# Kernel tuning notes

Hardware: AMD Instinct MI355X
Metric: run time of the kernel (lower is better)

Reference implementation:

```python
import jax, jax.numpy as jnp
import numpy as np

EPS = 1e-7
MAX_NORM = 10.0  # safe_expmap tangent-norm clamp


def _sinh_div(d):
    # sinh(d)/d, stable at d->0
    ds = jnp.maximum(d, 1e-6)
    return jnp.where(d < 1e-6, 1.0, jnp.sinh(ds) / ds)


def _div_sinh(d):
    # d/sinh(d), stable at d->0
    ds = jnp.maximum(d, 1e-6)
    return jnp.where(d < 1e-6, 1.0, ds / jnp.sinh(ds))


def projx(x):
    # re-project onto hyperboloid: x0 = sqrt(1 + ||x_spatial||^2)
    sp = x[..., 1:]
    x0 = jnp.sqrt(1.0 + jnp.sum(sp * sp, -1, keepdims=True))
    return jnp.concatenate([x0, sp], -1)


def logmap0(x):
    # log map at origin o=(1,0,...,0); tangent has first coord 0
    x0 = jnp.clip(x[..., :1], 1.0 + EPS, None)
    d = jnp.arccosh(x0)
    v_sp = _div_sinh(d) * x[..., 1:]
    return jnp.concatenate([jnp.zeros_like(x0), v_sp], -1)


def safe_expmap0(v):
    # exp map at origin with norm clamping for stability
    sp = v[..., 1:]
    n = jnp.sqrt(jnp.sum(sp * sp, -1, keepdims=True))
    scale = jnp.minimum(1.0, MAX_NORM / jnp.maximum(n, EPS))
    sp = sp * scale
    m = jnp.minimum(n, MAX_NORM)
    return jnp.concatenate([jnp.cosh(m), _sinh_div(m) * sp], -1)


def lorentz_inner(x, y):
    return -x[..., :1] * y[..., :1] + jnp.sum(x[..., 1:] * y[..., 1:], -1, keepdims=True)


def logmap(x, y):
    ip = jnp.clip(lorentz_inner(x, y), None, -(1.0 + EPS))
    d = jnp.arccosh(-ip)
    return _div_sinh(d) * (y + ip * x)


def safe_expmap(x, v):
    # exp map at x with Lorentz-norm clamping
    vv = lorentz_inner(v, v)
    n = jnp.sqrt(jnp.clip(vv, 0.0, None))
    scale = jnp.minimum(1.0, MAX_NORM / jnp.maximum(n, EPS))
    v = v * scale
    m = jnp.minimum(n, MAX_NORM)
    return jnp.cosh(m) * x + _sinh_div(m) * v


def lorentz_linear(x_hyp, W, b):
    # Lorentz -> tangent -> linear -> Lorentz
    y_tan = logmap0(x_hyp) @ W.T + b
    return projx(safe_expmap0(y_tan))


def setup_inputs() -> dict:
    key = jax.random.key(0)
    ks = jax.random.split(key, 8)
    N, D, H = 32768, 256, 1024
    z_sp = 0.5 * jax.random.normal(ks[0], (N, D - 1), dtype=jnp.float32)
    z_h = projx(jnp.concatenate([jnp.zeros((N, 1), jnp.float32), z_sp], -1))
    s = lambda fi, fo: (2.0 / (fi + fo)) ** 0.5
    return {
        "z_h": z_h,
        "w0": s(D, H) * jax.random.normal(ks[1], (H, D), dtype=jnp.float32),
        "b0": jnp.zeros((H,), jnp.float32),
        "w1": s(H, H) * jax.random.normal(ks[2], (H, H), dtype=jnp.float32),
        "b1": jnp.zeros((H,), jnp.float32),
        "w2": s(H, D) * jax.random.normal(ks[3], (D, H), dtype=jnp.float32),
        "b2": jnp.zeros((D,), jnp.float32),
        "alpha": jnp.float32(0.7),
        "step_size": jnp.float32(1.0),
    }


def reference(z_h, w0, b0, w1, b1, w2, b2, alpha, step_size):
    # v_tangent branch: x_previous is None, average_velocity is None
    v_tangent = logmap0(z_h)
    v_hyp = projx(safe_expmap0(v_tangent))

    # LorentzMLP (n_layers=2 -> 3 LorentzLinear layers); dropout is identity (eval)
    x = v_hyp
    for W, b in ((w0, b0), (w1, b1)):
        x = lorentz_linear(x, W, b)
        x = projx(safe_expmap0(logmap0(x)))
    v_transformed_hyp = lorentz_linear(x, w2, b2)

    v_transformed = logmap0(v_transformed_hyp)
    step = jax.nn.sigmoid(step_size)
    v_final = step * v_transformed
    z_update = projx(safe_expmap(z_h, v_final))

    a = jax.nn.sigmoid(alpha)
    tangent_direction = logmap(z_h, z_update)
    scaled_tangent = (1.0 - a) * tangent_direction
    z_next = projx(safe_expmap(z_h, scaled_tangent))
    return (z_next, z_h)
```

## Files before the change

### kernel.cpp

```cpp
#include <hip/hip_runtime.h>
#include <math.h>

#define EPSF 1e-7f
#define MAXN 10.0f

typedef unsigned short ushortT;
typedef __bf16 bf16_8 __attribute__((ext_vector_type(8)));
typedef float f32_4 __attribute__((ext_vector_type(4)));

#define MFMA16 __builtin_amdgcn_mfma_f32_16x16x32_bf16
#define BAR asm volatile("s_barrier" ::: "memory")

__device__ __forceinline__ float sinh_div_f(float d) {
    float ds = fmaxf(d, 1e-6f);
    return (d < 1e-6f) ? 1.0f : sinhf(ds) / ds;
}
__device__ __forceinline__ float div_sinh_f(float d) {
    float ds = fmaxf(d, 1e-6f);
    return (d < 1e-6f) ? 1.0f : ds / sinhf(ds);
}
__device__ __forceinline__ float wred(float v) {
#pragma unroll
    for (int off = 32; off > 0; off >>= 1) v += __shfl_xor(v, off, 64);
    return v;
}
__device__ __forceinline__ void bsplit(float x, ushortT& h, ushortT& l) {
    unsigned u = __float_as_uint(x);
    unsigned r = (u + 0x7fffu + ((u >> 16) & 1u)) >> 16;
    h = (ushortT)r;
    float lo = x - __uint_as_float(r << 16);
    unsigned ul = __float_as_uint(lo);
    l = (ushortT)((ul + 0x7fffu + ((ul >> 16) & 1u)) >> 16);
}
__device__ __forceinline__ void gload_lds16(const void* g, void* l) {
    __builtin_amdgcn_global_load_lds(
        (const __attribute__((address_space(1))) unsigned int*)g,
        (__attribute__((address_space(3))) unsigned int*)l, 16, 0, 0);
}

__global__ void split_kernel(const float* __restrict__ x, ushortT* __restrict__ hi,
                             ushortT* __restrict__ lo, int n4) {
    int idx = blockIdx.x * blockDim.x + threadIdx.x;
    if (idx >= n4) return;
    float4 v = reinterpret_cast<const float4*>(x)[idx];
    float f[4] = {v.x, v.y, v.z, v.w};
    ushortT hh[4], ll[4];
#pragma unroll
    for (int e = 0; e < 4; ++e) bsplit(f[e], hh[e], ll[e]);
    reinterpret_cast<ushort4*>(hi)[idx] = ushort4{hh[0], hh[1], hh[2], hh[3]};
    reinterpret_cast<ushort4*>(lo)[idx] = ushort4{ll[0], ll[1], ll[2], ll[3]};
}

__global__ void prep_kernel(const float* __restrict__ z, ushortT* __restrict__ th,
                            ushortT* __restrict__ tl, int N) {
    int gw = (blockIdx.x * blockDim.x + threadIdx.x) >> 6;
    int lane = threadIdx.x & 63;
    if (gw >= N) return;
    float4 zv = reinterpret_cast<const float4*>(z + (size_t)gw * 256)[lane];
    float z0 = __shfl(zv.x, 0, 64);
    float x0 = fmaxf(z0, 1.f + EPSF);
    float d = acoshf(x0);
    float f = div_sinh_f(d);
    float vx = (lane == 0) ? 0.f : zv.x * f;
    float vy = zv.y * f, vz = zv.z * f, vw = zv.w * f;
    float ss = wred(vx * vx + vy * vy + vz * vz + vw * vw);
    float n = sqrtf(ss);
    float s = fminf(1.f, MAXN / fmaxf(n, EPSF));
    float o[4] = {vx * s, vy * s, vz * s, vw * s};
    ushortT hh[4], ll[4];
#pragma unroll
    for (int e = 0; e < 4; ++e) bsplit(o[e], hh[e], ll[e]);
    reinterpret_cast<ushort4*>(th + (size_t)gw * 256)[lane] = ushort4{hh[0], hh[1], hh[2], hh[3]};
    reinterpret_cast<ushort4*>(tl + (size_t)gw * 256)[lane] = ushort4{ll[0], ll[1], ll[2], ll[3]};
}

__global__ void rowscale_kernel(const float* __restrict__ partials, float* __restrict__ scale,
                                int N, int nSlices) {
    int r = blockIdx.x * blockDim.x + threadIdx.x;
    if (r >= N) return;
    float s = 0.f;
    for (int k = 0; k < nSlices; ++k) s += partials[(size_t)k * N + r];
    float n = sqrtf(s);
    scale[r] = fminf(1.f, MAXN / fmaxf(n, EPSF));
}

template<int OUTMODE, int IM>
__global__ __launch_bounds__(512, 2) void gemm_v4(
    const ushortT* __restrict__ Ah_g, const ushortT* __restrict__ Al_g,
    const ushortT* __restrict__ Wh_g, const ushortT* __restrict__ Wl_g,
    const float* __restrict__ bias, const float* __restrict__ scaleA,
    float* __restrict__ outF, ushortT* __restrict__ outH, ushortT* __restrict__ outL,
    float* __restrict__ partials, int K, int M, int nColBlk, int Nrows)
{
    constexpr int BM = IM * 32;
    constexpr int AS = BM * 32;
    constexpr int BS = 256 * 32;
    constexpr int BUF = 2 * AS + 2 * BS;
    constexpr int HM = IM / 2;
    __shared__ __align__(16) ushortT lds[2 * BUF];

    const int tid = threadIdx.x;
    const int wid = tid >> 6, lane = tid & 63;
    const int nwg = gridDim.x;
    const int swz = ((int)blockIdx.x & 7) * (nwg >> 3) + ((int)blockIdx.x >> 3);
    const int rb = swz / nColBlk, cb = swz % nColBlk;
    const int rowBase = rb * BM, colBase = cb * 256;

    const int rl = tid >> 2;
    const int ks = (tid & 3) ^ ((rl >> 1) & 3);
    const int d8 = tid * 8;
    const ushortT* gAh0 = Ah_g + (size_t)(rowBase + rl) * K + ks * 8;
    const ushortT* gAl0 = Al_g + (size_t)(rowBase + rl) * K + ks * 8;
    const ushortT* gAh1 = Ah_g + (size_t)(rowBase + 128 + rl) * K + ks * 8;
    const ushortT* gAl1 = Al_g + (size_t)(rowBase + 128 + rl) * K + ks * 8;
    const ushortT* gBh0 = Wh_g + (size_t)(colBase + rl) * K + ks * 8;
    const ushortT* gBh1 = Wh_g + (size_t)(colBase + 128 + rl) * K + ks * 8;
    const ushortT* gBl0 = Wl_g + (size_t)(colBase + rl) * K + ks * 8;
    const ushortT* gBl1 = Wl_g + (size_t)(colBase + 128 + rl) * K + ks * 8;
#define STG(p, dst, nbo, nk) gload_lds16((p) + (nk), &lds[(nbo) + (dst) + d8])

    const int warpM = wid >> 2, warpN = wid & 3;
    const int frow = lane & 15, fk = lane >> 4;
    const int pslot8 = (fk ^ ((frow >> 1) & 3)) * 8;
    const int aoff = (warpM * (IM * 16) + frow) * 32 + pslot8;
    const int boff = (warpN * 64 + frow) * 32 + pslot8;

    f32_4 acc[IM][4];
#pragma unroll
    for (int i = 0; i < IM; ++i)
#pragma unroll
        for (int j = 0; j < 4; ++j) acc[i][j] = f32_4{0.f, 0.f, 0.f, 0.f};

    STG(gAh0, 0, 0, 0);
    if constexpr (IM == 8) STG(gAh1, 4096, 0, 0);
    STG(gAl0, AS, 0, 0);
    if constexpr (IM == 8) STG(gAl1, AS + 4096, 0, 0);
    STG(gBh0, 2 * AS, 0, 0); STG(gBh1, 2 * AS + 4096, 0, 0);
    STG(gBl0, 2 * AS + BS, 0, 0); STG(gBl1, 2 * AS + BS + 4096, 0, 0);
    asm volatile("s_waitcnt vmcnt(0)" ::: "memory");
    BAR;

    const int nt = K >> 5;
    for (int t = 0; t < nt; ++t) {
        const ushortT* lb = &lds[(t & 1) * BUF];
        const int nbo = ((t & 1) ^ 1) * BUF;
        const int nk = (t + 1) << 5;
        const bool more = (t + 1) < nt;
        bf16_8 ah[IM], bh[4], bl[4], alx[HM];

#pragma unroll
        for (int i = 0; i < HM; ++i) ah[i] = *reinterpret_cast<const bf16_8*>(&lb[aoff + i * 512]);
#pragma unroll
        for (int j = 0; j < 4; ++j) bh[j] = *reinterpret_cast<const bf16_8*>(&lb[2 * AS + boff + j * 512]);
        if (more) { STG(gAh0, 0, nbo, nk); if constexpr (IM == 8) STG(gAh1, 4096, nbo, nk); }
        BAR;
        __builtin_amdgcn_s_setprio(1);
#pragma unroll
        for (int i = 0; i < HM; ++i)
#pragma unroll
            for (int j = 0; j < 4; ++j) acc[i][j] = MFMA16(ah[i], bh[j], acc[i][j], 0, 0, 0);
        __builtin_amdgcn_s_setprio(0);

#pragma unroll
        for (int i = HM; i < IM; ++i) ah[i] = *reinterpret_cast<const bf16_8*>(&lb[aoff + i * 512]);
        if (more) { STG(gAl0, AS, nbo, nk); if constexpr (IM == 8) STG(gAl1, AS + 4096, nbo, nk); }
        BAR;
        __builtin_amdgcn_s_setprio(1);
#pragma unroll
        for (int i = HM; i < IM; ++i)
#pragma unroll
            for (int j = 0; j < 4; ++j) acc[i][j] = MFMA16(ah[i], bh[j], acc[i][j], 0, 0, 0);
        __builtin_amdgcn_s_setprio(0);

#pragma unroll
        for (int j = 0; j < 4; ++j) bl[j] = *reinterpret_cast<const bf16_8*>(&lb[2 * AS + BS + boff + j * 512]);
        if (more) { STG(gBh0, 2 * AS, nbo, nk); STG(gBh1, 2 * AS + 4096, nbo, nk); }
        BAR;
        __builtin_amdgcn_s_setprio(1);
#pragma unroll
        for (int i = 0; i < HM; ++i)
#pragma unroll
            for (int j = 0; j < 4; ++j) acc[i][j] = MFMA16(ah[i], bl[j], acc[i][j], 0, 0, 0);
        __builtin_amdgcn_s_setprio(0);

        if (more) { STG(gBl0, 2 * AS + BS, nbo, nk); STG(gBl1, 2 * AS + BS + 4096, nbo, nk); }
        BAR;
        __builtin_amdgcn_s_setprio(1);
#pragma unroll
        for (int i = HM; i < IM; ++i)
#pragma unroll
            for (int j = 0; j < 4; ++j) acc[i][j] = MFMA16(ah[i], bl[j], acc[i][j], 0, 0, 0);
        __builtin_amdgcn_s_setprio(0);

#pragma unroll
        for (int i = 0; i < HM; ++i) alx[i] = *reinterpret_cast<const bf16_8*>(&lb[AS + aoff + i * 512]);
        BAR;
        __builtin_amdgcn_s_setprio(1);
#pragma unroll
        for (int i = 0; i < HM; ++i)
#pragma unroll
            for (int j = 0; j < 4; ++j) acc[i][j] = MFMA16(alx[i], bh[j], acc[i][j], 0, 0, 0);
        __builtin_amdgcn_s_setprio(0);

#pragma unroll
        for (int i = 0; i < HM; ++i) alx[i] = *reinterpret_cast<const bf16_8*>(&lb[AS + aoff + (HM + i) * 512]);
        BAR;
        __builtin_amdgcn_s_setprio(1);
#pragma unroll
        for (int i = 0; i < HM; ++i)
#pragma unroll
            for (int j = 0; j < 4; ++j) acc[HM + i][j] = MFMA16(alx[i], bh[j], acc[HM + i][j], 0, 0, 0);
        __builtin_amdgcn_s_setprio(0);

        asm volatile("s_waitcnt vmcnt(0)" ::: "memory");
        BAR;
    }
#undef STG

    const int cbase = colBase + warpN * 64 + frow;
    if (OUTMODE == 0) {
        float bv[4];
#pragma unroll
        for (int j = 0; j < 4; ++j) bv[j] = bias[cbase + j * 16];
        const size_t slice = (size_t)(cb * 4 + warpN) * Nrows;
#pragma unroll
        for (int i = 0; i < IM; ++i) {
            const int row0 = rowBase + warpM * (IM * 16) + i * 16 + fk * 4;
            float4 sa4 = float4{1.f, 1.f, 1.f, 1.f};
            if (scaleA) sa4 = *reinterpret_cast<const float4*>(&scaleA[row0]);
            float psum[4];
#pragma unroll
            for (int r = 0; r < 4; ++r) {
                const float sa = reinterpret_cast<const float*>(&sa4)[r];
                const int row = row0 + r;
                const size_t base = (size_t)row * M;
                float ssv = 0.f;
#pragma unroll
                for (int j = 0; j < 4; ++j) {
                    float y = sa * acc[i][j][r] + bv[j];
                    if (j == 0 && cbase == 0) y = 0.f;
                    ushortT h, l;
                    bsplit(y, h, l);
                    outH[base + cbase + j * 16] = h;
                    outL[base + cbase + j * 16] = l;
                    ssv += y * y;
                }
                ssv += __shfl_xor(ssv, 1, 64); ssv += __shfl_xor(ssv, 2, 64);
                ssv += __shfl_xor(ssv, 4, 64); ssv += __shfl_xor(ssv, 8, 64);
                psum[r] = ssv;
            }
            if (frow == 0) {
#pragma unroll
                for (int r = 0; r < 4; ++r) partials[slice + row0 + r] = psum[r];
            }
        }
    } else {
#pragma unroll
        for (int i = 0; i < IM; ++i) {
            const int row0 = rowBase + warpM * (IM * 16) + i * 16 + fk * 4;
            float4 sa4 = float4{1.f, 1.f, 1.f, 1.f};
            if (scaleA) sa4 = *reinterpret_cast<const float4*>(&scaleA[row0]);
#pragma unroll
            for (int r = 0; r < 4; ++r) {
                const float sa = reinterpret_cast<const float*>(&sa4)[r];
                const size_t base = (size_t)(row0 + r) * M;
#pragma unroll
                for (int j = 0; j < 4; ++j)
                    outF[base + cbase + j * 16] = sa * acc[i][j][r] + bias[cbase + j * 16];
            }
        }
    }
}

__global__ void final_kernel(const float* __restrict__ y2buf, const float* __restrict__ z,
                             const float* __restrict__ alpha_p, const float* __restrict__ step_p,
                             float* __restrict__ out, int N) {
    int gw = (blockIdx.x * blockDim.x + threadIdx.x) >> 6;
    int lane = threadIdx.x & 63;
    if (gw >= N) return;
    const bool l0 = (lane == 0);

    float4 yv = reinterpret_cast<const float4*>(y2buf + (size_t)gw * 256)[lane];
    float4 zv = reinterpret_cast<const float4*>(z + (size_t)gw * 256)[lane];
    float z0 = __shfl(zv.x, 0, 64);

    float yx = l0 ? 0.f : yv.x;
    float ss2 = wred(yx * yx + yv.y * yv.y + yv.z * yv.z + yv.w * yv.w);
    float n2 = sqrtf(ss2);
    float s2 = fminf(1.f, MAXN / fmaxf(n2, EPSF));
    float step = 1.f / (1.f + expf(-step_p[0]));
    float k1 = s2 * step;
    float vfx = yx * k1, vfy = yv.y * k1, vfz = yv.z * k1, vfw = yv.w * k1;

    float r2 = wred(vfx * vfx + vfy * vfy + vfz * vfz + vfw * vfw);
    float n = sqrtf(fmaxf(r2, 0.f));
    float sc = fminf(1.f, MAXN / fmaxf(n, EPSF));
    float m = fminf(n, MAXN);
    float ch = coshf(m), sd = sinh_div_f(m);
    float ex = ch * zv.x + sd * sc * vfx;
    float ey = ch * zv.y + sd * sc * vfy;
    float ez = ch * zv.z + sd * sc * vfz;
    float ew = ch * zv.w + sd * sc * vfw;
    float exq = l0 ? 0.f : ex;
    float r3 = wred(exq * exq + ey * ey + ez * ez + ew * ew);
    float u0 = sqrtf(1.f + r3);

    float r4 = wred((l0 ? 0.f : zv.x * ex) + zv.y * ey + zv.z * ez + zv.w * ew);
    float ip = r4 - z0 * u0;
    ip = fminf(ip, -(1.f + EPSF));
    float dd = acoshf(-ip);
    float g = div_sinh_f(dd);
    float a = 1.f / (1.f + expf(-alpha_p[0]));
    float oa = (1.f - a) * g;
    float st0 = oa * (u0 + ip * z0);
    float stx = oa * (ex + ip * zv.x);
    float sty = oa * (ey + ip * zv.y);
    float stz = oa * (ez + ip * zv.z);
    float stw = oa * (ew + ip * zv.w);
    float stxq = l0 ? 0.f : stx;

    float r5 = wred(stxq * stxq + sty * sty + stz * stz + stw * stw);
    float vv2 = r5 - st0 * st0;
    float n5 = sqrtf(fmaxf(vv2, 0.f));
    float s5 = fminf(1.f, MAXN / fmaxf(n5, EPSF));
    float m5 = fminf(n5, MAXN);
    float ch5 = coshf(m5), sd5 = sinh_div_f(m5);
    float fx = ch5 * zv.x + sd5 * s5 * stxq;
    float fy = ch5 * zv.y + sd5 * s5 * sty;
    float fz = ch5 * zv.z + sd5 * s5 * stz;
    float fw = ch5 * zv.w + sd5 * s5 * stw;
    float fxq = l0 ? 0.f : fx;
    float r6 = wred(fxq * fxq + fy * fy + fz * fz + fw * fw);
    float zn0 = sqrtf(1.f + r6);
    if (l0) fx = zn0;

    float4 o;
    o.x = fx; o.y = fy; o.z = fz; o.w = fw;
    reinterpret_cast<float4*>(out + (size_t)gw * 256)[lane] = o;
    reinterpret_cast<float4*>(out + ((size_t)N + gw) * 256)[lane] = zv;
}

extern "C" void kernel_launch(void* const* d_in, const int* in_sizes, int n_in,
                              void* d_out, int out_size, void* d_ws, size_t ws_size,
                              hipStream_t stream) {
    const float* z_h  = (const float*)d_in[0];
    const float* w0   = (const float*)d_in[1];
    const float* b0   = (const float*)d_in[2];
    const float* w1   = (const float*)d_in[3];
    const float* b1   = (const float*)d_in[4];
    const float* w2   = (const float*)d_in[5];
    const float* b2   = (const float*)d_in[6];
    const float* alph = (const float*)d_in[7];
    const float* stps = (const float*)d_in[8];
    float* out = (float*)d_out;

    const int D = 256, H = 1024;
    const int N = in_sizes[0] / D;

    char* arena = (char*)d_out;
    ushortT* w0h = (ushortT*)(arena + 0);
    ushortT* w0l = (ushortT*)(arena + 524288);
    ushortT* w1h = (ushortT*)(arena + 1048576);
    ushortT* w1l = (ushortT*)(arena + 3145728);
    ushortT* w2h = (ushortT*)(arena + 5242880);
    ushortT* w2l = (ushortT*)(arena + 5767168);
    float* partials = (float*)(arena + 6291456);
    float* s1 = (float*)(arena + 10485760);
    float* s2 = (float*)(arena + 10616832);
    ushortT* p0h = (ushortT*)(arena + 10747904);
    ushortT* p0l = (ushortT*)(arena + 27525120);

    ushortT* paH = (ushortT*)d_ws;
    ushortT* paL = paH + (size_t)N * H;
    ushortT* pbH = paL + (size_t)N * H;
    ushortT* pbL = pbH + (size_t)N * H;
    float* y2F = (float*)d_ws;

    split_kernel<<<(H * D / 4 + 255) / 256, 256, 0, stream>>>(w0, w0h, w0l, H * D / 4);
    split_kernel<<<(H * H / 4 + 255) / 256, 256, 0, stream>>>(w1, w1h, w1l, H * H / 4);
    split_kernel<<<(D * H / 4 + 255) / 256, 256, 0, stream>>>(w2, w2h, w2l, D * H / 4);

    prep_kernel<<<N / 4, 256, 0, stream>>>(z_h, p0h, p0l, N);

    gemm_v4<0, 8><<<(N / 256) * (H / 256), 512, 0, stream>>>(
        p0h, p0l, w0h, w0l, b0, nullptr, nullptr, paH, paL, partials, D, H, H / 256, N);
    rowscale_kernel<<<(N + 255) / 256, 256, 0, stream>>>(partials, s1, N, 16);

    gemm_v4<0, 8><<<(N / 256) * (H / 256), 512, 0, stream>>>(
        paH, paL, w1h, w1l, b1, s1, nullptr, pbH, pbL, partials, H, H, H / 256, N);
    rowscale_kernel<<<(N + 255) / 256, 256, 0, stream>>>(partials, s2, N, 16);

    gemm_v4<1, 4><<<(N / 128) * (D / 256), 512, 0, stream>>>(
        pbH, pbL, w2h, w2l, b2, s2, y2F, nullptr, nullptr, nullptr, H, D, D / 256, N);

    final_kernel<<<N / 4, 256, 0, stream>>>(y2F, z_h, alph, stps, out, N);
}
```

Measured before the change: 381.5 us.

## Switch split-bf16 GEMMs from 16x16x32 to 32x32x16 MFMA tiles

Replaces the 16x16x32 bf16 MFMA fragments in the three-way split-precision GEMM with 32x32x16 MFMA, changing the fragment loading, the accumulator layout and the epilogue row/column mapping. The larger MFMA tile reuses each LDS-loaded fragment for more output, which cuts LDS read traffic and instruction count per FLOP. The K=32 step is now split into two k-halves, with a new interleaving of barriers and global-to-LDS prefetches. The epilogue's row-norm partial reduction is rewritten for the 32-lane column layout, which risks more shuffles and less coalesced stores.

```diff
diff --git a/kernel.cpp b/kernel.cpp
--- a/kernel.cpp
+++ b/kernel.cpp
@@ -6,9 +6,9 @@
 
 typedef unsigned short ushortT;
 typedef __bf16 bf16_8 __attribute__((ext_vector_type(8)));
-typedef float f32_4 __attribute__((ext_vector_type(4)));
-
-#define MFMA16 __builtin_amdgcn_mfma_f32_16x16x32_bf16
+typedef float f32_16 __attribute__((ext_vector_type(16)));
+
+#define MFMA32 __builtin_amdgcn_mfma_f32_32x32x16_bf16
 #define BAR asm volatile("s_barrier" ::: "memory")
 
 __device__ __forceinline__ float sinh_div_f(float d) {
@@ -36,6 +36,10 @@
     __builtin_amdgcn_global_load_lds(
         (const __attribute__((address_space(1))) unsigned int*)g,
         (__attribute__((address_space(3))) unsigned int*)l, 16, 0, 0);
+}
+__device__ __forceinline__ bf16_8 fragld(const ushortT* p, int row, int kk, int lh) {
+    int slot = ((kk << 1) | lh) ^ ((row >> 1) & 3);
+    return *reinterpret_cast<const bf16_8*>(&p[row * 32 + slot * 8]);
 }
 
 __global__ void split_kernel(const float* __restrict__ x, ushortT* __restrict__ hi,
@@ -85,7 +89,7 @@
 }
 
 template<int OUTMODE, int IM>
-__global__ __launch_bounds__(512, 2) void gemm_v4(
+__global__ __launch_bounds__(512, 2) void gemm_v5(
     const ushortT* __restrict__ Ah_g, const ushortT* __restrict__ Al_g,
     const ushortT* __restrict__ Wh_g, const ushortT* __restrict__ Wl_g,
     const float* __restrict__ bias, const float* __restrict__ scaleA,
@@ -93,10 +97,10 @@
     float* __restrict__ partials, int K, int M, int nColBlk, int Nrows)
 {
     constexpr int BM = IM * 32;
+    constexpr int MT = IM / 2;
     constexpr int AS = BM * 32;
     constexpr int BS = 256 * 32;
     constexpr int BUF = 2 * AS + 2 * BS;
-    constexpr int HM = IM / 2;
     __shared__ __align__(16) ushortT lds[2 * BUF];
 
     const int tid = threadIdx.x;
@@ -120,16 +124,17 @@
 #define STG(p, dst, nbo, nk) gload_lds16((p) + (nk), &lds[(nbo) + (dst) + d8])
 
     const int warpM = wid >> 2, warpN = wid & 3;
-    const int frow = lane & 15, fk = lane >> 4;
-    const int pslot8 = (fk ^ ((frow >> 1) & 3)) * 8;
-    const int aoff = (warpM * (IM * 16) + frow) * 32 + pslot8;
-    const int boff = (warpN * 64 + frow) * 32 + pslot8;
-
-    f32_4 acc[IM][4];
-#pragma unroll
-    for (int i = 0; i < IM; ++i)
-#pragma unroll
-        for (int j = 0; j < 4; ++j) acc[i][j] = f32_4{0.f, 0.f, 0.f, 0.f};
+    const int l31 = lane & 31, lh = lane >> 5;
+    const int arow0 = warpM * (IM * 16) + l31;
+    const int brow0 = warpN * 64 + l31;
+
+    f32_16 acc[MT][2];
+#pragma unroll
+    for (int m = 0; m < MT; ++m)
+#pragma unroll
+        for (int n = 0; n < 2; ++n)
+#pragma unroll
+            for (int r = 0; r < 16; ++r) acc[m][n][r] = 0.f;
 
     STG(gAh0, 0, 0, 0);
     if constexpr (IM == 8) STG(gAh1, 4096, 0, 0);
@@ -146,127 +151,141 @@
         const int nbo = ((t & 1) ^ 1) * BUF;
         const int nk = (t + 1) << 5;
         const bool more = (t + 1) < nt;
-        bf16_8 ah[IM], bh[4], bl[4], alx[HM];
-
-#pragma unroll
-        for (int i = 0; i < HM; ++i) ah[i] = *reinterpret_cast<const bf16_8*>(&lb[aoff + i * 512]);
-#pragma unroll
-        for (int j = 0; j < 4; ++j) bh[j] = *reinterpret_cast<const bf16_8*>(&lb[2 * AS + boff + j * 512]);
-        if (more) { STG(gAh0, 0, nbo, nk); if constexpr (IM == 8) STG(gAh1, 4096, nbo, nk); }
-        BAR;
-        __builtin_amdgcn_s_setprio(1);
-#pragma unroll
-        for (int i = 0; i < HM; ++i)
-#pragma unroll
-            for (int j = 0; j < 4; ++j) acc[i][j] = MFMA16(ah[i], bh[j], acc[i][j], 0, 0, 0);
-        __builtin_amdgcn_s_setprio(0);
-
-#pragma unroll
-        for (int i = HM; i < IM; ++i) ah[i] = *reinterpret_cast<const bf16_8*>(&lb[aoff + i * 512]);
-        if (more) { STG(gAl0, AS, nbo, nk); if constexpr (IM == 8) STG(gAl1, AS + 4096, nbo, nk); }
-        BAR;
-        __builtin_amdgcn_s_setprio(1);
-#pragma unroll
-        for (int i = HM; i < IM; ++i)
-#pragma unroll
-            for (int j = 0; j < 4; ++j) acc[i][j] = MFMA16(ah[i], bh[j], acc[i][j], 0, 0, 0);
-        __builtin_amdgcn_s_setprio(0);
-
-#pragma unroll
-        for (int j = 0; j < 4; ++j) bl[j] = *reinterpret_cast<const bf16_8*>(&lb[2 * AS + BS + boff + j * 512]);
+        const ushortT* lAh = lb;
+        const ushortT* lAl = lb + AS;
+        const ushortT* lBh = lb + 2 * AS;
+        const ushortT* lBl = lb + 2 * AS + BS;
+
+        bf16_8 ah0[MT], ah1[MT], bh0[2], bh1[2], bl0[2], bl1[2], al0[MT], al1[MT];
+
+#pragma unroll
+        for (int m = 0; m < MT; ++m) ah0[m] = fragld(lAh, arow0 + m * 32, 0, lh);
+        bh0[0] = fragld(lBh, brow0, 0, lh);
+        bh0[1] = fragld(lBh, brow0 + 32, 0, lh);
+        if (more) {
+            STG(gAh0, 0, nbo, nk);
+            if constexpr (IM == 8) STG(gAh1, 4096, nbo, nk);
+        }
+        BAR;
+#pragma unroll
+        for (int m = 0; m < MT; ++m) ah1[m] = fragld(lAh, arow0 + m * 32, 1, lh);
+        bh1[0] = fragld(lBh, brow0, 1, lh);
+        bh1[1] = fragld(lBh, brow0 + 32, 1, lh);
+        __builtin_amdgcn_s_setprio(1);
+#pragma unroll
+        for (int m = 0; m < MT; ++m) {
+            acc[m][0] = MFMA32(ah0[m], bh0[0], acc[m][0], 0, 0, 0);
+            acc[m][1] = MFMA32(ah0[m], bh0[1], acc[m][1], 0, 0, 0);
+        }
+        __builtin_amdgcn_s_setprio(0);
+        BAR;
+        bl0[0] = fragld(lBl, brow0, 0, lh);
+        bl0[1] = fragld(lBl, brow0 + 32, 0, lh);
+        if (more) {
+            STG(gAl0, AS, nbo, nk);
+            if constexpr (IM == 8) STG(gAl1, AS + 4096, nbo, nk);
+        }
+        __builtin_amdgcn_s_setprio(1);
+#pragma unroll
+        for (int m = 0; m < MT; ++m) {
+            acc[m][0] = MFMA32(ah1[m], bh1[0], acc[m][0], 0, 0, 0);
+            acc[m][1] = MFMA32(ah1[m], bh1[1], acc[m][1], 0, 0, 0);
+        }
+        __builtin_amdgcn_s_setprio(0);
+        BAR;
+        bl1[0] = fragld(lBl, brow0, 1, lh);
+        bl1[1] = fragld(lBl, brow0 + 32, 1, lh);
         if (more) { STG(gBh0, 2 * AS, nbo, nk); STG(gBh1, 2 * AS + 4096, nbo, nk); }
-        BAR;
-        __builtin_amdgcn_s_setprio(1);
-#pragma unroll
-        for (int i = 0; i < HM; ++i)
-#pragma unroll
-            for (int j = 0; j < 4; ++j) acc[i][j] = MFMA16(ah[i], bl[j], acc[i][j], 0, 0, 0);
-        __builtin_amdgcn_s_setprio(0);
-
+        __builtin_amdgcn_s_setprio(1);
+#pragma unroll
+        for (int m = 0; m < MT; ++m) {
+            acc[m][0] = MFMA32(ah0[m], bl0[0], acc[m][0], 0, 0, 0);
+            acc[m][1] = MFMA32(ah0[m], bl0[1], acc[m][1], 0, 0, 0);
+        }
+        __builtin_amdgcn_s_setprio(0);
+        BAR;
+#pragma unroll
+        for (int m = 0; m < MT; ++m) al0[m] = fragld(lAl, arow0 + m * 32, 0, lh);
         if (more) { STG(gBl0, 2 * AS + BS, nbo, nk); STG(gBl1, 2 * AS + BS + 4096, nbo, nk); }
-        BAR;
-        __builtin_amdgcn_s_setprio(1);
-#pragma unroll
-        for (int i = HM; i < IM; ++i)
-#pragma unroll
-            for (int j = 0; j < 4; ++j) acc[i][j] = MFMA16(ah[i], bl[j], acc[i][j], 0, 0, 0);
-        __builtin_amdgcn_s_setprio(0);
-
-#pragma unroll
-        for (int i = 0; i < HM; ++i) alx[i] = *reinterpret_cast<const bf16_8*>(&lb[AS + aoff + i * 512]);
-        BAR;
-        __builtin_amdgcn_s_setprio(1);
-#pragma unroll
-        for (int i = 0; i < HM; ++i)
-#pragma unroll
-            for (int j = 0; j < 4; ++j) acc[i][j] = MFMA16(alx[i], bh[j], acc[i][j], 0, 0, 0);
-        __builtin_amdgcn_s_setprio(0);
-
-#pragma unroll
-        for (int i = 0; i < HM; ++i) alx[i] = *reinterpret_cast<const bf16_8*>(&lb[AS + aoff + (HM + i) * 512]);
-        BAR;
-        __builtin_amdgcn_s_setprio(1);
-#pragma unroll
-        for (int i = 0; i < HM; ++i)
-#pragma unroll
-            for (int j = 0; j < 4; ++j) acc[HM + i][j] = MFMA16(alx[i], bh[j], acc[HM + i][j], 0, 0, 0);
-        __builtin_amdgcn_s_setprio(0);
-
+        __builtin_amdgcn_s_setprio(1);
+#pragma unroll
+        for (int m = 0; m < MT; ++m) {
+            acc[m][0] = MFMA32(ah1[m], bl1[0], acc[m][0], 0, 0, 0);
+            acc[m][1] = MFMA32(ah1[m], bl1[1], acc[m][1], 0, 0, 0);
+        }
+        __builtin_amdgcn_s_setprio(0);
+        BAR;
+#pragma unroll
+        for (int m = 0; m < MT; ++m) al1[m] = fragld(lAl, arow0 + m * 32, 1, lh);
+        __builtin_amdgcn_s_setprio(1);
+#pragma unroll
+        for (int m = 0; m < MT; ++m) {
+            acc[m][0] = MFMA32(al0[m], bh0[0], acc[m][0], 0, 0, 0);
+            acc[m][1] = MFMA32(al0[m], bh0[1], acc[m][1], 0, 0, 0);
+        }
+        __builtin_amdgcn_s_setprio(0);
+        BAR;
+        __builtin_amdgcn_s_setprio(1);
+#pragma unroll
+        for (int m = 0; m < MT; ++m) {
+            acc[m][0] = MFMA32(al1[m], bh1[0], acc[m][0], 0, 0, 0);
+            acc[m][1] = MFMA32(al1[m], bh1[1], acc[m][1], 0, 0, 0);
+        }
+        __builtin_amdgcn_s_setprio(0);
         asm volatile("s_waitcnt vmcnt(0)" ::: "memory");
         BAR;
     }
 #undef STG
 
-    const int cbase = colBase + warpN * 64 + frow;
+    const int cbase = colBase + warpN * 64 + l31;
+    float bv[2] = {bias[cbase], bias[cbase + 32]};
     if (OUTMODE == 0) {
-        float bv[4];
-#pragma unroll
-        for (int j = 0; j < 4; ++j) bv[j] = bias[cbase + j * 16];
         const size_t slice = (size_t)(cb * 4 + warpN) * Nrows;
 #pragma unroll
-        for (int i = 0; i < IM; ++i) {
-            const int row0 = rowBase + warpM * (IM * 16) + i * 16 + fk * 4;
-            float4 sa4 = float4{1.f, 1.f, 1.f, 1.f};
-            if (scaleA) sa4 = *reinterpret_cast<const float4*>(&scaleA[row0]);
-            float psum[4];
-#pragma unroll
-            for (int r = 0; r < 4; ++r) {
-                const float sa = reinterpret_cast<const float*>(&sa4)[r];
-                const int row = row0 + r;
-                const size_t base = (size_t)row * M;
-                float ssv = 0.f;
-#pragma unroll
-                for (int j = 0; j < 4; ++j) {
-                    float y = sa * acc[i][j][r] + bv[j];
-                    if (j == 0 && cbase == 0) y = 0.f;
-                    ushortT h, l;
-                    bsplit(y, h, l);
-                    outH[base + cbase + j * 16] = h;
-                    outL[base + cbase + j * 16] = l;
-                    ssv += y * y;
+        for (int m = 0; m < MT; ++m) {
+            const int rbase = rowBase + warpM * (IM * 16) + m * 32 + 4 * lh;
+#pragma unroll
+            for (int q = 0; q < 4; ++q) {
+                float4 sa4 = float4{1.f, 1.f, 1.f, 1.f};
+                if (scaleA) sa4 = *reinterpret_cast<const float4*>(&scaleA[rbase + q * 8]);
+#pragma unroll
+                for (int rr = 0; rr < 4; ++rr) {
+                    const int r = q * 4 + rr;
+                    const int row = rbase + q * 8 + rr;
+                    const float sa = reinterpret_cast<const float*>(&sa4)[rr];
+                    float y0 = sa * acc[m][0][r] + bv[0];
+                    if (cbase == 0) y0 = 0.f;
+                    float y1 = sa * acc[m][1][r] + bv[1];
+                    ushortT h0, l0, h1, l1;
+                    bsplit(y0, h0, l0); bsplit(y1, h1, l1);
+                    const size_t base = (size_t)row * M;
+                    outH[base + cbase] = h0; outH[base + cbase + 32] = h1;
+                    outL[base + cbase] = l0; outL[base + cbase + 32] = l1;
+                    float ssv = y0 * y0 + y1 * y1;
+                    ssv += __shfl_xor(ssv, 1, 64); ssv += __shfl_xor(ssv, 2, 64);
+                    ssv += __shfl_xor(ssv, 4, 64); ssv += __shfl_xor(ssv, 8, 64);
+                    ssv += __shfl_xor(ssv, 16, 64);
+                    if (l31 == 0) partials[slice + row] = ssv;
                 }
-                ssv += __shfl_xor(ssv, 1, 64); ssv += __shfl_xor(ssv, 2, 64);
-                ssv += __shfl_xor(ssv, 4, 64); ssv += __shfl_xor(ssv, 8, 64);
-                psum[r] = ssv;
             }
-            if (frow == 0) {
-#pragma unroll
-                for (int r = 0; r < 4; ++r) partials[slice + row0 + r] = psum[r];
-            }
         }
     } else {
 #pragma unroll
-        for (int i = 0; i < IM; ++i) {
-            const int row0 = rowBase + warpM * (IM * 16) + i * 16 + fk * 4;
-            float4 sa4 = float4{1.f, 1.f, 1.f, 1.f};
-            if (scaleA) sa4 = *reinterpret_cast<const float4*>(&scaleA[row0]);
-#pragma unroll
-            for (int r = 0; r < 4; ++r) {
-                const float sa = reinterpret_cast<const float*>(&sa4)[r];
-                const size_t base = (size_t)(row0 + r) * M;
-#pragma unroll
-                for (int j = 0; j < 4; ++j)
-                    outF[base + cbase + j * 16] = sa * acc[i][j][r] + bias[cbase + j * 16];
+        for (int m = 0; m < MT; ++m) {
+            const int rbase = rowBase + warpM * (IM * 16) + m * 32 + 4 * lh;
+#pragma unroll
+            for (int q = 0; q < 4; ++q) {
+                float4 sa4 = float4{1.f, 1.f, 1.f, 1.f};
+                if (scaleA) sa4 = *reinterpret_cast<const float4*>(&scaleA[rbase + q * 8]);
+#pragma unroll
+                for (int rr = 0; rr < 4; ++rr) {
+                    const int r = q * 4 + rr;
+                    const int row = rbase + q * 8 + rr;
+                    const float sa = reinterpret_cast<const float*>(&sa4)[rr];
+                    const size_t base = (size_t)row * M;
+                    outF[base + cbase]      = sa * acc[m][0][r] + bv[0];
+                    outF[base + cbase + 32] = sa * acc[m][1][r] + bv[1];
+                }
             }
         }
     }
@@ -382,15 +401,15 @@
 
     prep_kernel<<<N / 4, 256, 0, stream>>>(z_h, p0h, p0l, N);
 
-    gemm_v4<0, 8><<<(N / 256) * (H / 256), 512, 0, stream>>>(
+    gemm_v5<0, 8><<<(N / 256) * (H / 256), 512, 0, stream>>>(
         p0h, p0l, w0h, w0l, b0, nullptr, nullptr, paH, paL, partials, D, H, H / 256, N);
     rowscale_kernel<<<(N + 255) / 256, 256, 0, stream>>>(partials, s1, N, 16);
 
-    gemm_v4<0, 8><<<(N / 256) * (H / 256), 512, 0, stream>>>(
+    gemm_v5<0, 8><<<(N / 256) * (H / 256), 512, 0, stream>>>(
         paH, paL, w1h, w1l, b1, s1, nullptr, pbH, pbL, partials, H, H, H / 256, N);
     rowscale_kernel<<<(N + 255) / 256, 256, 0, stream>>>(partials, s2, N, 16);
 
-    gemm_v4<1, 4><<<(N / 128) * (D / 256), 512, 0, stream>>>(
+    gemm_v5<1, 4><<<(N / 128) * (D / 256), 512, 0, stream>>>(
         pbH, pbL, w2h, w2l, b2, s2, y2F, nullptr, nullptr, nullptr, H, D, D / 256, N);
 
     final_kernel<<<N / 4, 256, 0, stream>>>(y2F, z_h, alph, stps, out, N);
```

New measurement: 428.0 us. 1.12x slower.

## Fuse final hyperbolic update into last GEMM epilogue and merge prep kernels

Applied to the files above, without the earlier changes.

Moves the whole final_kernel computation (expmap, logmap, second expmap, projection) into the epilogue of the last GEMM, using LDS for the cross-warp row reductions, so the fp32 y2 intermediate is never written to or read back from global memory. It also merges the weight-split kernels with the prep and rowscale kernels to cut launch count, and relaxes the vmcnt waits in the GEMM main loop so more loads stay in flight. The trade-offs are extra barriers and register pressure in the epilogue, plus a reshuffled workspace and output arena layout.

```diff
diff --git a/kernel.cpp b/kernel.cpp
--- a/kernel.cpp
+++ b/kernel.cpp
@@ -22,6 +22,11 @@
 __device__ __forceinline__ float wred(float v) {
 #pragma unroll
     for (int off = 32; off > 0; off >>= 1) v += __shfl_xor(v, off, 64);
+    return v;
+}
+__device__ __forceinline__ float red16(float v) {
+    v += __shfl_xor(v, 1, 64); v += __shfl_xor(v, 2, 64);
+    v += __shfl_xor(v, 4, 64); v += __shfl_xor(v, 8, 64);
     return v;
 }
 __device__ __forceinline__ void bsplit(float x, ushortT& h, ushortT& l) {
@@ -37,11 +42,9 @@
         (const __attribute__((address_space(1))) unsigned int*)g,
         (__attribute__((address_space(3))) unsigned int*)l, 16, 0, 0);
 }
-
-__global__ void split_kernel(const float* __restrict__ x, ushortT* __restrict__ hi,
-                             ushortT* __restrict__ lo, int n4) {
-    int idx = blockIdx.x * blockDim.x + threadIdx.x;
-    if (idx >= n4) return;
+__device__ __forceinline__ void split_item(const float* __restrict__ x,
+                                           ushortT* __restrict__ hi, ushortT* __restrict__ lo,
+                                           int idx) {
     float4 v = reinterpret_cast<const float4*>(x)[idx];
     float f[4] = {v.x, v.y, v.z, v.w};
     ushortT hh[4], ll[4];
@@ -51,10 +54,22 @@
     reinterpret_cast<ushort4*>(lo)[idx] = ushort4{ll[0], ll[1], ll[2], ll[3]};
 }
 
-__global__ void prep_kernel(const float* __restrict__ z, ushortT* __restrict__ th,
-                            ushortT* __restrict__ tl, int N) {
-    int gw = (blockIdx.x * blockDim.x + threadIdx.x) >> 6;
-    int lane = threadIdx.x & 63;
+__global__ void combo1(const float* __restrict__ z, const float* __restrict__ w0,
+                       const float* __restrict__ w1,
+                       ushortT* __restrict__ p0h, ushortT* __restrict__ p0l,
+                       ushortT* __restrict__ w0h, ushortT* __restrict__ w0l,
+                       ushortT* __restrict__ w1h, ushortT* __restrict__ w1l, int N) {
+    int b = blockIdx.x, tid = threadIdx.x;
+    if (b < 256) {
+        split_item(w0, w0h, w0l, b * 256 + tid);
+        return;
+    }
+    if (b < 1280) {
+        split_item(w1, w1h, w1l, (b - 256) * 256 + tid);
+        return;
+    }
+    int gw = (b - 1280) * 4 + (tid >> 6);
+    int lane = tid & 63;
     if (gw >= N) return;
     float4 zv = reinterpret_cast<const float4*>(z + (size_t)gw * 256)[lane];
     float z0 = __shfl(zv.x, 0, 64);
@@ -70,8 +85,8 @@
     ushortT hh[4], ll[4];
 #pragma unroll
     for (int e = 0; e < 4; ++e) bsplit(o[e], hh[e], ll[e]);
-    reinterpret_cast<ushort4*>(th + (size_t)gw * 256)[lane] = ushort4{hh[0], hh[1], hh[2], hh[3]};
-    reinterpret_cast<ushort4*>(tl + (size_t)gw * 256)[lane] = ushort4{ll[0], ll[1], ll[2], ll[3]};
+    reinterpret_cast<ushort4*>(p0h + (size_t)gw * 256)[lane] = ushort4{hh[0], hh[1], hh[2], hh[3]};
+    reinterpret_cast<ushort4*>(p0l + (size_t)gw * 256)[lane] = ushort4{ll[0], ll[1], ll[2], ll[3]};
 }
 
 __global__ void rowscale_kernel(const float* __restrict__ partials, float* __restrict__ scale,
@@ -84,13 +99,31 @@
     scale[r] = fminf(1.f, MAXN / fmaxf(n, EPSF));
 }
 
+__global__ void combo2(const float* __restrict__ partials, float* __restrict__ s2,
+                       const float* __restrict__ w2,
+                       ushortT* __restrict__ w2h, ushortT* __restrict__ w2l, int N) {
+    int b = blockIdx.x, tid = threadIdx.x;
+    if (b < 128) {
+        int r = b * 256 + tid;
+        if (r >= N) return;
+        float s = 0.f;
+        for (int k = 0; k < 16; ++k) s += partials[(size_t)k * N + r];
+        float n = sqrtf(s);
+        s2[r] = fminf(1.f, MAXN / fmaxf(n, EPSF));
+        return;
+    }
+    split_item(w2, w2h, w2l, (b - 128) * 256 + tid);
+}
+
 template<int OUTMODE, int IM>
-__global__ __launch_bounds__(512, 2) void gemm_v4(
+__global__ __launch_bounds__(512, 2) void gemm_v7(
     const ushortT* __restrict__ Ah_g, const ushortT* __restrict__ Al_g,
     const ushortT* __restrict__ Wh_g, const ushortT* __restrict__ Wl_g,
     const float* __restrict__ bias, const float* __restrict__ scaleA,
     float* __restrict__ outF, ushortT* __restrict__ outH, ushortT* __restrict__ outL,
-    float* __restrict__ partials, int K, int M, int nColBlk, int Nrows)
+    float* __restrict__ partials, int K, int M, int nColBlk, int Nrows,
+    const float* __restrict__ z_g, const float* __restrict__ alpha_p,
+    const float* __restrict__ step_p)
 {
     constexpr int BM = IM * 32;
     constexpr int AS = BM * 32;
@@ -163,7 +196,14 @@
 
 #pragma unroll
         for (int i = HM; i < IM; ++i) ah[i] = *reinterpret_cast<const bf16_8*>(&lb[aoff + i * 512]);
-        if (more) { STG(gAl0, AS, nbo, nk); if constexpr (IM == 8) STG(gAl1, AS + 4096, nbo, nk); }
+        if (more) {
+            STG(gAl0, AS, nbo, nk);
+            if constexpr (IM == 8) STG(gAl1, AS + 4096, nbo, nk);
+            if constexpr (IM == 8) asm volatile("s_waitcnt vmcnt(4)" ::: "memory");
+            else                   asm volatile("s_waitcnt vmcnt(2)" ::: "memory");
+        } else {
+            asm volatile("s_waitcnt vmcnt(0)" ::: "memory");
+        }
         BAR;
         __builtin_amdgcn_s_setprio(1);
 #pragma unroll
@@ -212,13 +252,13 @@
             for (int j = 0; j < 4; ++j) acc[HM + i][j] = MFMA16(alx[i], bh[j], acc[HM + i][j], 0, 0, 0);
         __builtin_amdgcn_s_setprio(0);
 
-        asm volatile("s_waitcnt vmcnt(0)" ::: "memory");
+        asm volatile("s_waitcnt vmcnt(2)" ::: "memory");
         BAR;
     }
 #undef STG
 
     const int cbase = colBase + warpN * 64 + frow;
-    if (OUTMODE == 0) {
+    if constexpr (OUTMODE == 0) {
         float bv[4];
 #pragma unroll
         for (int j = 0; j < 4; ++j) bv[j] = bias[cbase + j * 16];
@@ -245,99 +285,163 @@
                     outL[base + cbase + j * 16] = l;
                     ssv += y * y;
                 }
-                ssv += __shfl_xor(ssv, 1, 64); ssv += __shfl_xor(ssv, 2, 64);
-                ssv += __shfl_xor(ssv, 4, 64); ssv += __shfl_xor(ssv, 8, 64);
-                psum[r] = ssv;
+                psum[r] = red16(ssv);
             }
             if (frow == 0) {
 #pragma unroll
                 for (int r = 0; r < 4; ++r) partials[slice + row0 + r] = psum[r];
             }
         }
-    } else {
-#pragma unroll
-        for (int i = 0; i < IM; ++i) {
-            const int row0 = rowBase + warpM * (IM * 16) + i * 16 + fk * 4;
-            float4 sa4 = float4{1.f, 1.f, 1.f, 1.f};
-            if (scaleA) sa4 = *reinterpret_cast<const float4*>(&scaleA[row0]);
-#pragma unroll
-            for (int r = 0; r < 4; ++r) {
-                const float sa = reinterpret_cast<const float*>(&sa4)[r];
-                const size_t base = (size_t)(row0 + r) * M;
-#pragma unroll
-                for (int j = 0; j < 4; ++j)
-                    outF[base + cbase + j * 16] = sa * acc[i][j][r] + bias[cbase + j * 16];
+    }
+    if constexpr (OUTMODE == 2) {
+        float* red  = (float*)&lds[0];
+        float* bufZ = red;
+        float* bufA = red + 128;
+        float* bufB = red + 640;
+        float* bufC = red + 1664;
+        float* bufD = red + 2176;
+        const float stepv = 1.f / (1.f + expf(-step_p[0]));
+        const float av    = 1.f / (1.f + expf(-alpha_p[0]));
+        const int cb0 = warpN * 64 + frow;
+        const bool c0own = (cb0 == 0);
+        float bv[4];
+#pragma unroll
+        for (int j = 0; j < 4; ++j) bv[j] = bias[cb0 + j * 16];
+        BAR;
+#pragma unroll
+        for (int ig = 0; ig < 2; ++ig) {
+            float yv[2][4][4], zz[2][4][4], z0[2][4], st0[2][4];
+#pragma unroll
+            for (int ii = 0; ii < 2; ++ii) {
+                const int i = ig * 2 + ii;
+                const int row0 = warpM * 64 + i * 16 + fk * 4;
+                float4 sa4 = float4{1.f, 1.f, 1.f, 1.f};
+                if (scaleA) sa4 = *reinterpret_cast<const float4*>(&scaleA[rowBase + row0]);
+#pragma unroll
+                for (int rr = 0; rr < 4; ++rr) {
+                    const float sa = reinterpret_cast<const float*>(&sa4)[rr];
+                    const size_t gz = (size_t)(rowBase + row0 + rr) * 256 + cb0;
+#pragma unroll
+                    for (int j = 0; j < 4; ++j) {
+                        yv[ii][j][rr] = sa * acc[i][j][rr] + bv[j];
+                        zz[ii][j][rr] = z_g[gz + j * 16];
+                    }
+                }
+            }
+#pragma unroll
+            for (int ii = 0; ii < 2; ++ii) {
+                const int row0 = warpM * 64 + (ig * 2 + ii) * 16 + fk * 4;
+#pragma unroll
+                for (int rr = 0; rr < 4; ++rr) {
+                    float p = 0.f;
+#pragma unroll
+                    for (int j = 0; j < 4; ++j) {
+                        float yq = (c0own && j == 0) ? 0.f : yv[ii][j][rr];
+                        p += yq * yq;
+                    }
+                    p = red16(p);
+                    if (frow == 0) bufA[(row0 + rr) * 4 + warpN] = p;
+                    if (c0own) bufZ[row0 + rr] = zz[ii][0][rr];
+                }
+            }
+            BAR;
+#pragma unroll
+            for (int ii = 0; ii < 2; ++ii) {
+                const int row0 = warpM * 64 + (ig * 2 + ii) * 16 + fk * 4;
+#pragma unroll
+                for (int rr = 0; rr < 4; ++rr) {
+                    const int rw = row0 + rr;
+                    float ss2 = bufA[rw * 4] + bufA[rw * 4 + 1] + bufA[rw * 4 + 2] + bufA[rw * 4 + 3];
+                    z0[ii][rr] = bufZ[rw];
+                    float n2 = sqrtf(ss2);
+                    float k1 = fminf(1.f, MAXN / fmaxf(n2, EPSF)) * stepv;
+                    float n  = k1 * n2;
+                    float scv = fminf(1.f, MAXN / fmaxf(n, EPSF));
+                    float m  = fminf(n, MAXN);
+                    float ch = coshf(m), sdv = sinh_div_f(m);
+                    float pe = 0.f, pz = 0.f;
+#pragma unroll
+                    for (int j = 0; j < 4; ++j) {
+                        float vf = (c0own && j == 0) ? 0.f : yv[ii][j][rr] * k1;
+                        float e  = ch * zz[ii][j][rr] + sdv * scv * vf;
+                        yv[ii][j][rr] = e;
+                        if (!(c0own && j == 0)) { pe += e * e; pz += zz[ii][j][rr] * e; }
+                    }
+                    pe = red16(pe); pz = red16(pz);
+                    if (frow == 0) { bufB[rw * 8 + warpN * 2] = pe; bufB[rw * 8 + warpN * 2 + 1] = pz; }
+                }
+            }
+            BAR;
+#pragma unroll
+            for (int ii = 0; ii < 2; ++ii) {
+                const int row0 = warpM * 64 + (ig * 2 + ii) * 16 + fk * 4;
+#pragma unroll
+                for (int rr = 0; rr < 4; ++rr) {
+                    const int rw = row0 + rr;
+                    float r3 = bufB[rw * 8] + bufB[rw * 8 + 2] + bufB[rw * 8 + 4] + bufB[rw * 8 + 6];
+                    float r4 = bufB[rw * 8 + 1] + bufB[rw * 8 + 3] + bufB[rw * 8 + 5] + bufB[rw * 8 + 7];
+                    float u0 = sqrtf(1.f + r3);
+                    float ip = fminf(r4 - z0[ii][rr] * u0, -(1.f + EPSF));
+                    float dd = acoshf(-ip);
+                    float g = div_sinh_f(dd);
+                    float oa = (1.f - av) * g;
+                    st0[ii][rr] = oa * (u0 + ip * z0[ii][rr]);
+                    float p5 = 0.f;
+#pragma unroll
+                    for (int j = 0; j < 4; ++j) {
+                        float st = oa * (yv[ii][j][rr] + ip * zz[ii][j][rr]);
+                        yv[ii][j][rr] = st;
+                        if (!(c0own && j == 0)) p5 += st * st;
+                    }
+                    p5 = red16(p5);
+                    if (frow == 0) bufC[rw * 4 + warpN] = p5;
+                }
+            }
+            BAR;
+#pragma unroll
+            for (int ii = 0; ii < 2; ++ii) {
+                const int row0 = warpM * 64 + (ig * 2 + ii) * 16 + fk * 4;
+#pragma unroll
+                for (int rr = 0; rr < 4; ++rr) {
+                    const int rw = row0 + rr;
+                    float r5 = bufC[rw * 4] + bufC[rw * 4 + 1] + bufC[rw * 4 + 2] + bufC[rw * 4 + 3];
+                    float vv2 = r5 - st0[ii][rr] * st0[ii][rr];
+                    float n5 = sqrtf(fmaxf(vv2, 0.f));
+                    float s5 = fminf(1.f, MAXN / fmaxf(n5, EPSF));
+                    float m5 = fminf(n5, MAXN);
+                    float ch5 = coshf(m5), sd5 = sinh_div_f(m5);
+                    float p6 = 0.f;
+#pragma unroll
+                    for (int j = 0; j < 4; ++j) {
+                        float f = ch5 * zz[ii][j][rr] + sd5 * s5 * yv[ii][j][rr];
+                        yv[ii][j][rr] = f;
+                        if (!(c0own && j == 0)) p6 += f * f;
+                    }
+                    p6 = red16(p6);
+                    if (frow == 0) bufD[rw * 4 + warpN] = p6;
+                }
+            }
+            BAR;
+#pragma unroll
+            for (int ii = 0; ii < 2; ++ii) {
+                const int row0 = warpM * 64 + (ig * 2 + ii) * 16 + fk * 4;
+#pragma unroll
+                for (int rr = 0; rr < 4; ++rr) {
+                    const int rw = row0 + rr;
+                    float r6 = bufD[rw * 4] + bufD[rw * 4 + 1] + bufD[rw * 4 + 2] + bufD[rw * 4 + 3];
+                    float zn0 = sqrtf(1.f + r6);
+                    const size_t rowG = (size_t)(rowBase + rw);
+#pragma unroll
+                    for (int j = 0; j < 4; ++j) {
+                        const int col = cb0 + j * 16;
+                        float v = (c0own && j == 0) ? zn0 : yv[ii][j][rr];
+                        outF[rowG * 256 + col] = v;
+                        outF[((size_t)Nrows + rowG) * 256 + col] = zz[ii][j][rr];
+                    }
+                }
             }
         }
     }
-}
-
-__global__ void final_kernel(const float* __restrict__ y2buf, const float* __restrict__ z,
-                             const float* __restrict__ alpha_p, const float* __restrict__ step_p,
-                             float* __restrict__ out, int N) {
-    int gw = (blockIdx.x * blockDim.x + threadIdx.x) >> 6;
-    int lane = threadIdx.x & 63;
-    if (gw >= N) return;
-    const bool l0 = (lane == 0);
-
-    float4 yv = reinterpret_cast<const float4*>(y2buf + (size_t)gw * 256)[lane];
-    float4 zv = reinterpret_cast<const float4*>(z + (size_t)gw * 256)[lane];
-    float z0 = __shfl(zv.x, 0, 64);
-
-    float yx = l0 ? 0.f : yv.x;
-    float ss2 = wred(yx * yx + yv.y * yv.y + yv.z * yv.z + yv.w * yv.w);
-    float n2 = sqrtf(ss2);
-    float s2 = fminf(1.f, MAXN / fmaxf(n2, EPSF));
-    float step = 1.f / (1.f + expf(-step_p[0]));
-    float k1 = s2 * step;
-    float vfx = yx * k1, vfy = yv.y * k1, vfz = yv.z * k1, vfw = yv.w * k1;
-
-    float r2 = wred(vfx * vfx + vfy * vfy + vfz * vfz + vfw * vfw);
-    float n = sqrtf(fmaxf(r2, 0.f));
-    float sc = fminf(1.f, MAXN / fmaxf(n, EPSF));
-    float m = fminf(n, MAXN);
-    float ch = coshf(m), sd = sinh_div_f(m);
-    float ex = ch * zv.x + sd * sc * vfx;
-    float ey = ch * zv.y + sd * sc * vfy;
-    float ez = ch * zv.z + sd * sc * vfz;
-    float ew = ch * zv.w + sd * sc * vfw;
-    float exq = l0 ? 0.f : ex;
-    float r3 = wred(exq * exq + ey * ey + ez * ez + ew * ew);
-    float u0 = sqrtf(1.f + r3);
-
-    float r4 = wred((l0 ? 0.f : zv.x * ex) + zv.y * ey + zv.z * ez + zv.w * ew);
-    float ip = r4 - z0 * u0;
-    ip = fminf(ip, -(1.f + EPSF));
-    float dd = acoshf(-ip);
-    float g = div_sinh_f(dd);
-    float a = 1.f / (1.f + expf(-alpha_p[0]));
-    float oa = (1.f - a) * g;
-    float st0 = oa * (u0 + ip * z0);
-    float stx = oa * (ex + ip * zv.x);
-    float sty = oa * (ey + ip * zv.y);
-    float stz = oa * (ez + ip * zv.z);
-    float stw = oa * (ew + ip * zv.w);
-    float stxq = l0 ? 0.f : stx;
-
-    float r5 = wred(stxq * stxq + sty * sty + stz * stz + stw * stw);
-    float vv2 = r5 - st0 * st0;
-    float n5 = sqrtf(fmaxf(vv2, 0.f));
-    float s5 = fminf(1.f, MAXN / fmaxf(n5, EPSF));
-    float m5 = fminf(n5, MAXN);
-    float ch5 = coshf(m5), sd5 = sinh_div_f(m5);
-    float fx = ch5 * zv.x + sd5 * s5 * stxq;
-    float fy = ch5 * zv.y + sd5 * s5 * sty;
-    float fz = ch5 * zv.z + sd5 * s5 * stz;
-    float fw = ch5 * zv.w + sd5 * s5 * stw;
-    float fxq = l0 ? 0.f : fx;
-    float r6 = wred(fxq * fxq + fy * fy + fz * fz + fw * fw);
-    float zn0 = sqrtf(1.f + r6);
-    if (l0) fx = zn0;
-
-    float4 o;
-    o.x = fx; o.y = fy; o.z = fz; o.w = fw;
-    reinterpret_cast<float4*>(out + (size_t)gw * 256)[lane] = o;
-    reinterpret_cast<float4*>(out + ((size_t)N + gw) * 256)[lane] = zv;
 }
 
 extern "C" void kernel_launch(void* const* d_in, const int* in_sizes, int n_in,
@@ -357,41 +461,39 @@
     const int D = 256, H = 1024;
     const int N = in_sizes[0] / D;
 
-    char* arena = (char*)d_out;
-    ushortT* w0h = (ushortT*)(arena + 0);
-    ushortT* w0l = (ushortT*)(arena + 524288);
-    ushortT* w1h = (ushortT*)(arena + 1048576);
-    ushortT* w1l = (ushortT*)(arena + 3145728);
-    ushortT* w2h = (ushortT*)(arena + 5242880);
-    ushortT* w2l = (ushortT*)(arena + 5767168);
-    float* partials = (float*)(arena + 6291456);
-    float* s1 = (float*)(arena + 10485760);
-    float* s2 = (float*)(arena + 10616832);
-    ushortT* p0h = (ushortT*)(arena + 10747904);
-    ushortT* p0l = (ushortT*)(arena + 27525120);
+    char* ob = (char*)d_out;
+    ushortT* p0h = (ushortT*)ob;
+    ushortT* p0l = (ushortT*)(ob + 16777216);
+    char* s2b = ob + 33554432;
+    ushortT* w0h = (ushortT*)(s2b);
+    ushortT* w0l = (ushortT*)(s2b + 524288);
+    ushortT* w1h = (ushortT*)(s2b + 1048576);
+    ushortT* w1l = (ushortT*)(s2b + 3145728);
+    float* partials = (float*)(s2b + 5242880);
+    float* s1 = (float*)(s2b + 7340032);
 
     ushortT* paH = (ushortT*)d_ws;
     ushortT* paL = paH + (size_t)N * H;
     ushortT* pbH = paL + (size_t)N * H;
     ushortT* pbL = pbH + (size_t)N * H;
-    float* y2F = (float*)d_ws;
-
-    split_kernel<<<(H * D / 4 + 255) / 256, 256, 0, stream>>>(w0, w0h, w0l, H * D / 4);
-    split_kernel<<<(H * H / 4 + 255) / 256, 256, 0, stream>>>(w1, w1h, w1l, H * H / 4);
-    split_kernel<<<(D * H / 4 + 255) / 256, 256, 0, stream>>>(w2, w2h, w2l, D * H / 4);
-
-    prep_kernel<<<N / 4, 256, 0, stream>>>(z_h, p0h, p0l, N);
-
-    gemm_v4<0, 8><<<(N / 256) * (H / 256), 512, 0, stream>>>(
-        p0h, p0l, w0h, w0l, b0, nullptr, nullptr, paH, paL, partials, D, H, H / 256, N);
+    ushortT* w2h = (ushortT*)d_ws;
+    ushortT* w2l = (ushortT*)((char*)d_ws + 524288);
+    float* s2 = (float*)((char*)d_ws + 1048576);
+
+    combo1<<<1280 + N / 4, 256, 0, stream>>>(z_h, w0, w1, p0h, p0l, w0h, w0l, w1h, w1l, N);
+
+    gemm_v7<0, 8><<<(N / 256) * (H / 256), 512, 0, stream>>>(
+        p0h, p0l, w0h, w0l, b0, nullptr, nullptr, paH, paL, partials, D, H, H / 256, N,
+        nullptr, nullptr, nullptr);
     rowscale_kernel<<<(N + 255) / 256, 256, 0, stream>>>(partials, s1, N, 16);
 
-    gemm_v4<0, 8><<<(N / 256) * (H / 256), 512, 0, stream>>>(
-        paH, paL, w1h, w1l, b1, s1, nullptr, pbH, pbL, partials, H, H, H / 256, N);
-    rowscale_kernel<<<(N + 255) / 256, 256, 0, stream>>>(partials, s2, N, 16);
-
-    gemm_v4<1, 4><<<(N / 128) * (D / 256), 512, 0, stream>>>(
-        pbH, pbL, w2h, w2l, b2, s2, y2F, nullptr, nullptr, nullptr, H, D, D / 256, N);
-
-    final_kernel<<<N / 4, 256, 0, stream>>>(y2F, z_h, alph, stps, out, N);
-}
+    gemm_v7<0, 8><<<(N / 256) * (H / 256), 512, 0, stream>>>(
+        paH, paL, w1h, w1l, b1, s1, nullptr, pbH, pbL, partials, H, H, H / 256, N,
+        nullptr, nullptr, nullptr);
+
+    combo2<<<384, 256, 0, stream>>>(partials, s2, w2, w2h, w2l, N);
+
+    gemm_v7<2, 4><<<(N / 128) * (D / 256), 512, 0, stream>>>(
+        pbH, pbL, w2h, w2l, b2, s2, out, nullptr, nullptr, nullptr, H, D, D / 256, N,
+        z_h, alph, stps);
+}
```

New measurement: 391.1 us. +2.5%, slower.
